# Performance work log

Measured on AMD Instinct MI355X. Metric: run time of the kernel, lower is better.

The kernel has to match this reference:

```python
import jax, jax.numpy as jnp
import numpy as np

EMB = 768
HEADS = 12


def setup_inputs() -> dict:
    key = jax.random.key(0)
    ks = jax.random.split(key, 5)
    B, N, E = 8, 1024, EMB
    x = jax.random.normal(ks[0], (B, N, E), dtype=jnp.float32)
    s = 1.0 / np.sqrt(E)
    W_qkv = jax.random.normal(ks[1], (E, 3 * E), dtype=jnp.float32) * s
    b_qkv = jnp.zeros((3 * E,), dtype=jnp.float32)
    W_fc = jax.random.normal(ks[2], (E, E), dtype=jnp.float32) * s
    b_fc = jnp.zeros((E,), dtype=jnp.float32)
    return {"x": x, "W_qkv": W_qkv, "b_qkv": b_qkv, "W_fc": W_fc, "b_fc": b_fc}


def reference(x, W_qkv, b_qkv, W_fc, b_fc):
    B, N, E = x.shape
    H = HEADS
    D = E // H
    qkv = x @ W_qkv + b_qkv                      # [B, N, 3E]
    q, k, v = jnp.split(qkv, 3, axis=-1)
    # b n (h d) -> b h n d
    def to_heads(t):
        return t.reshape(B, N, H, D).transpose(0, 2, 1, 3)
    q, k, v = to_heads(q), to_heads(k), to_heads(v)
    scale = 1.0 / jnp.sqrt(jnp.float32(E))       # NOTE: scales by sqrt(emb_size), not head dim
    attn = jnp.einsum('bhid,bhjd->bhij', q, k) * scale
    attn = jax.nn.softmax(attn, axis=-1)
    out = jnp.einsum('bhij,bhjd->bhid', attn, v)
    out = out.transpose(0, 2, 1, 3).reshape(B, N, E)  # b h n d -> b n (h d)
    return out @ W_fc + b_fc
```

## Files before the change

### kernel.cpp

```cpp
#include <hip/hip_runtime.h>
#include <hip/hip_bf16.h>


typedef unsigned short u16;
typedef unsigned int u32;
typedef __attribute__((ext_vector_type(8))) short short8;
typedef __attribute__((ext_vector_type(4))) float f32x4;

#define DEV static __device__ __forceinline__

DEV u16 f2bf(float f) {
  union { float f; u32 u; } v; v.f = f;
  return (u16)((v.u + 0x7FFFu + ((v.u >> 16) & 1u)) >> 16);
}

DEV u32 pk2(float lo, float hi) {
  union { __hip_bfloat162 h2; u32 u; } v;
  v.h2.x = __float2bfloat16(lo);
  v.h2.y = __float2bfloat16(hi);
  return v.u;
}

DEV void gload_lds16(const void* g, void* l) {
  __builtin_amdgcn_global_load_lds(
      (const __attribute__((address_space(1))) void*)g,
      (__attribute__((address_space(3))) void*)l, 16, 0, 0);
}

__global__ void prep_kernel(const float* __restrict__ x, u16* __restrict__ xb,
                            const float* __restrict__ Wq, u16* __restrict__ WqT,
                            const float* __restrict__ Wf, u16* __restrict__ WfT) {
  __shared__ u16 tile[64][72];
  const int b = blockIdx.x;
  const int t = threadIdx.x;
  if (b < 576) {
    const float* in;
    u16* out;
    int Nn, bid;
    if (b < 432) { in = Wq; out = WqT; Nn = 2304; bid = b; }
    else         { in = Wf; out = WfT; Nn = 768;  bid = b - 432; }
    const int K = 768;
    int ntiles = Nn >> 6;
    int tk = bid / ntiles, tn = bid % ntiles;
    int k0 = tk << 6, n0 = tn << 6;
    int r = t >> 4;
    int c4 = (t & 15) << 2;
#pragma unroll
    for (int ps = 0; ps < 4; ++ps) {
      int k = r + ps * 16;
      float4 v = *reinterpret_cast<const float4*>(&in[(size_t)(k0 + k) * Nn + n0 + c4]);
      tile[c4 + 0][k] = f2bf(v.x);
      tile[c4 + 1][k] = f2bf(v.y);
      tile[c4 + 2][k] = f2bf(v.z);
      tile[c4 + 3][k] = f2bf(v.w);
    }
    __syncthreads();
    int nr = t >> 3;
    int c8 = (t & 7) << 3;
#pragma unroll
    for (int ps = 0; ps < 2; ++ps) {
      int n = nr + ps * 32;
      uint4 v = *reinterpret_cast<const uint4*>(&tile[n][c8]);
      *reinterpret_cast<uint4*>(&out[(size_t)(n0 + n) * K + k0 + c8]) = v;
    }
  } else {
    const int n8 = (8192 * 768) / 8;
    int idx = (b - 576) * 256 + t;
    const int stride = 2048 * 256;
    for (int i = idx; i < n8; i += stride) {
      float4 a = reinterpret_cast<const float4*>(x)[2 * i];
      float4 c = reinterpret_cast<const float4*>(x)[2 * i + 1];
      uint4 o;
      o.x = f2bf(a.x) | ((u32)f2bf(a.y) << 16);
      o.y = f2bf(a.z) | ((u32)f2bf(a.w) << 16);
      o.z = f2bf(c.x) | ((u32)f2bf(c.y) << 16);
      o.w = f2bf(c.z) | ((u32)f2bf(c.w) << 16);
      reinterpret_cast<uint4*>(xb)[i] = o;
    }
  }
}

template <int MODE>
__global__ __launch_bounds__(256, 4) void gemm_bt(
    const u16* __restrict__ A, const u16* __restrict__ Bt,
    const float* __restrict__ bias, void* __restrict__ Cout,
    u16* __restrict__ qh, u16* __restrict__ kh, u16* __restrict__ vt,
    int Nn) {
  __shared__ u16 SMEM[17408];
  u16* const As0 = SMEM;
  u16* const As1 = SMEM + 4096;
  u16* const Bs0 = SMEM + 8192;
  u16* const Bs1 = SMEM + 12288;
  const int nTn = Nn >> 7;
  const int nwg = gridDim.x;
  int wg = blockIdx.x;
  wg = (wg & 7) * (nwg >> 3) + (wg >> 3);
  const int tm = wg / nTn, tn = wg % nTn;
  const int m0 = tm << 7, n0 = tn << 7;
  const int tid = threadIdx.x;
  const int w = tid >> 6, lane = tid & 63;
  const int g = lane >> 4, p = lane & 15;
  const int wr = w >> 1, wc = w & 1;

  const int srow = lane >> 2;
  const int schunk = (lane & 3) ^ ((srow >> 1) & 3);
  const u16* Asrc = A + (size_t)(m0 + srow) * 768 + schunk * 8;
  const u16* Bsrc = Bt + (size_t)(n0 + srow) * 768 + schunk * 8;
  const int csw = (g ^ ((p >> 1) & 3)) << 3;

  f32x4 acc[4][4] = {};

#define STAGE(kt, ap, bp)                                                       \
  do {                                                                          \
    _Pragma("unroll")                                                           \
    for (int i = 0; i < 2; ++i) {                                               \
      int trow = w * 32 + i * 16;                                               \
      gload_lds16(Asrc + (size_t)trow * 768 + (kt) * 32, (ap) + trow * 32);     \
      gload_lds16(Bsrc + (size_t)trow * 768 + (kt) * 32, (bp) + trow * 32);     \
    }                                                                           \
  } while (0)

  STAGE(0, As0, Bs0);
  __syncthreads();

  int buf = 0;
  for (int k = 0; k < 24; ++k) {
    const u16* as = buf ? As1 : As0;
    const u16* bs = buf ? Bs1 : Bs0;
    short8 af[4], bf[4];
#pragma unroll
    for (int mb = 0; mb < 4; ++mb)
      af[mb] = *reinterpret_cast<const short8*>(&as[(wr * 64 + mb * 16 + p) * 32 + csw]);
#pragma unroll
    for (int nb = 0; nb < 4; ++nb)
      bf[nb] = *reinterpret_cast<const short8*>(&bs[(wc * 64 + nb * 16 + p) * 32 + csw]);
    if (k < 23) STAGE(k + 1, buf ? As0 : As1, buf ? Bs0 : Bs1);
#pragma unroll
    for (int mb = 0; mb < 4; ++mb)
#pragma unroll
      for (int nb = 0; nb < 4; ++nb)
        acc[mb][nb] = __builtin_amdgcn_mfma_f32_16x16x32_bf16(af[mb], bf[nb], acc[mb][nb], 0, 0, 0);
    __syncthreads();
    buf ^= 1;
  }
#undef STAGE

  const float qscale = 0.05205878290161879f;
  if (MODE == 0) {
#pragma unroll
    for (int nb = 0; nb < 4; ++nb) {
      int ncol = n0 + wc * 64 + nb * 16 + p;
      float bv = bias[ncol];
#pragma unroll
      for (int mb = 0; mb < 4; ++mb)
#pragma unroll
        for (int r = 0; r < 4; ++r) {
          int m = m0 + wr * 64 + mb * 16 + g * 4 + r;
          ((float*)Cout)[(size_t)m * Nn + ncol] = acc[mb][nb][r] + bv;
        }
    }
  } else if (n0 < 1536) {
#pragma unroll
    for (int nb = 0; nb < 4; ++nb) {
      int ncol = n0 + wc * 64 + nb * 16 + p;
      float bv = bias[ncol];
      int h64 = ncol >> 6;
      int which = h64 / 12;
      int hh = h64 - which * 12;
      int d = ncol & 63;
      u16* dst = which == 0 ? qh : kh;
      float sc = which == 0 ? qscale : 1.f;
#pragma unroll
      for (int mb = 0; mb < 4; ++mb)
#pragma unroll
        for (int r = 0; r < 4; ++r) {
          int m = m0 + wr * 64 + mb * 16 + g * 4 + r;
          int bb = m >> 10, nr = m & 1023;
          dst[(((size_t)bb * 12 + hh) * 1024 + nr) * 64 + d] = f2bf((acc[mb][nb][r] + bv) * sc);
        }
    }
  } else {
#pragma unroll
    for (int nb = 0; nb < 4; ++nb) {
      int nl = wc * 64 + nb * 16 + p;
      float bv = bias[n0 + nl];
#pragma unroll
      for (int mb = 0; mb < 4; ++mb) {
        int mlb = wr * 64 + mb * 16 + g * 4;
        uint2 pkv;
        pkv.x = (u32)f2bf(acc[mb][nb][0] + bv) | ((u32)f2bf(acc[mb][nb][1] + bv) << 16);
        pkv.y = (u32)f2bf(acc[mb][nb][2] + bv) | ((u32)f2bf(acc[mb][nb][3] + bv) << 16);
        *reinterpret_cast<uint2*>(&SMEM[nl * 136 + mlb]) = pkv;
      }
    }
    __syncthreads();
    const int hhb = (n0 - 1536) >> 6;
    const int bb = m0 >> 10;
    const int nseq0 = m0 & 1023;
    const int c16 = (tid & 7) * 16;
#pragma unroll
    for (int ps = 0; ps < 4; ++ps) {
      int nl = (tid >> 3) + ps * 32;
      int hh = hhb + (nl >> 6);
      int d = nl & 63;
      u16* dst = vt + (((size_t)(bb * 12 + hh) * 64 + d) << 10) + nseq0 + c16;
      uint4 v0 = *reinterpret_cast<const uint4*>(&SMEM[nl * 136 + c16]);
      uint4 v1 = *reinterpret_cast<const uint4*>(&SMEM[nl * 136 + c16 + 8]);
      *reinterpret_cast<uint4*>(dst) = v0;
      *reinterpret_cast<uint4*>(dst + 8) = v1;
    }
  }
}

__global__ __launch_bounds__(512, 6) void attn_kernel(
    const u16* __restrict__ qh, const u16* __restrict__ kh,
    const u16* __restrict__ vt, u16* __restrict__ ao) {
  __shared__ u16 Ks[2][64 * 64];
  __shared__ u16 Vs[2][64 * 64];
  __shared__ u16 Ps[8][16 * 64];
  const int bid = blockIdx.x;
  const int qt = bid & 7;
  const int bh = bid >> 3;
  const int b = bh / 12, h = bh % 12;
  const int tid = threadIdx.x;
  const int w = tid >> 6, lane = tid & 63;
  const int g = lane >> 4, p = lane & 15;
  const int qrow = qt * 128 + w * 16;

  const u16* qbase = qh + ((size_t)bh * 1024 + qrow + p) * 64;
  short8 qf0 = *reinterpret_cast<const short8*>(qbase + g * 8);
  short8 qf1 = *reinterpret_cast<const short8*>(qbase + 32 + g * 8);

  const int ci = w * 64 + lane;
  const int crow = ci >> 3;
  const int csw = (ci & 7) ^ (crow & 7);
  const u16* ksrc = kh + (((size_t)bh * 1024 + crow) << 6) + csw * 8;
  const u16* vsrc = vt + ((size_t)bh * 64 + crow) * 1024 + csw * 8;
  u16* myp = Ps[w];

  const int sw = p & 7;
  const int c0 = (g ^ sw) << 3;
  const int c1 = ((4 + g) ^ sw) << 3;

  float m_run = -1e30f, l_run = 0.f;
  f32x4 oacc[4] = {};

  gload_lds16(ksrc, &Ks[0][w * 512]);
  gload_lds16(vsrc, &Vs[0][w * 512]);
  __syncthreads();

  int buf = 0;
  for (int kt = 0; kt < 1024; kt += 64) {
    if (kt < 960) {
      gload_lds16(ksrc + ((kt + 64) << 6), &Ks[buf ^ 1][w * 512]);
      gload_lds16(vsrc + (kt + 64), &Vs[buf ^ 1][w * 512]);
    }

    f32x4 s[4];
    __builtin_amdgcn_s_setprio(1);
#pragma unroll
    for (int jb = 0; jb < 4; ++jb) {
      const u16* kb = &Ks[buf][(jb * 16 + p) * 64];
      short8 k0 = *reinterpret_cast<const short8*>(kb + c0);
      short8 k1 = *reinterpret_cast<const short8*>(kb + c1);
      f32x4 z = {};
      z = __builtin_amdgcn_mfma_f32_16x16x32_bf16(k0, qf0, z, 0, 0, 0);
      z = __builtin_amdgcn_mfma_f32_16x16x32_bf16(k1, qf1, z, 0, 0, 0);
      s[jb] = z;
    }
    __builtin_amdgcn_s_setprio(0);

    float tmax = -1e30f;
#pragma unroll
    for (int jb = 0; jb < 4; ++jb)
#pragma unroll
      for (int r = 0; r < 4; ++r) tmax = fmaxf(tmax, s[jb][r]);
    tmax = fmaxf(tmax, __shfl_xor(tmax, 16));
    tmax = fmaxf(tmax, __shfl_xor(tmax, 32));

    if (!__all(tmax - m_run <= 8.f)) {
      float m_new = fmaxf(m_run, tmax);
      float alpha = __builtin_amdgcn_exp2f(m_run - m_new);
      float al[4];
#pragma unroll
      for (int r = 0; r < 4; ++r) al[r] = __shfl(alpha, g * 4 + r);
#pragma unroll
      for (int nb = 0; nb < 4; ++nb)
#pragma unroll
        for (int r = 0; r < 4; ++r) oacc[nb][r] *= al[r];
      l_run *= alpha;
      m_run = m_new;
    }

    float lsum = 0.f;
#pragma unroll
    for (int jb = 0; jb < 4; ++jb)
#pragma unroll
      for (int r = 0; r < 4; ++r) {
        float e = __builtin_amdgcn_exp2f(s[jb][r] - m_run);
        s[jb][r] = e;
        lsum += e;
      }
    lsum += __shfl_xor(lsum, 16);
    lsum += __shfl_xor(lsum, 32);
    l_run += lsum;

#pragma unroll
    for (int jb = 0; jb < 4; ++jb) {
      uint2 pkv;
      pkv.x = pk2(s[jb][0], s[jb][1]);
      pkv.y = pk2(s[jb][2], s[jb][3]);
      int c = 2 * jb + (g >> 1);
      *reinterpret_cast<uint2*>(&myp[p * 64 + ((c ^ sw) << 3) + ((g & 1) << 2)]) = pkv;
    }

    short8 pa0 = *reinterpret_cast<const short8*>(&myp[p * 64 + c0]);
    short8 pa1 = *reinterpret_cast<const short8*>(&myp[p * 64 + c1]);
    __builtin_amdgcn_s_setprio(1);
#pragma unroll
    for (int nb = 0; nb < 4; ++nb) {
      const u16* vb = &Vs[buf][(nb * 16 + p) * 64];
      short8 v0 = *reinterpret_cast<const short8*>(vb + c0);
      short8 v1 = *reinterpret_cast<const short8*>(vb + c1);
      oacc[nb] = __builtin_amdgcn_mfma_f32_16x16x32_bf16(pa0, v0, oacc[nb], 0, 0, 0);
      oacc[nb] = __builtin_amdgcn_mfma_f32_16x16x32_bf16(pa1, v1, oacc[nb], 0, 0, 0);
    }
    __builtin_amdgcn_s_setprio(0);

    __syncthreads();
    buf ^= 1;
  }

  float li[4];
#pragma unroll
  for (int r = 0; r < 4; ++r) li[r] = 1.f / __shfl(l_run, g * 4 + r);
  u16* obase = ao + ((size_t)(b * 1024 + qrow)) * 768 + h * 64;
#pragma unroll
  for (int nb = 0; nb < 4; ++nb)
#pragma unroll
    for (int r = 0; r < 4; ++r)
      obase[(size_t)(g * 4 + r) * 768 + nb * 16 + p] = f2bf(oacc[nb][r] * li[r]);
}

extern "C" void kernel_launch(void* const* d_in, const int* in_sizes, int n_in,
                              void* d_out, int out_size, void* d_ws, size_t ws_size,
                              hipStream_t stream) {
  const float* x = (const float*)d_in[0];
  const float* Wqkv = (const float*)d_in[1];
  const float* bqkv = (const float*)d_in[2];
  const float* Wfc = (const float*)d_in[3];
  const float* bfc = (const float*)d_in[4];
  float* out = (float*)d_out;

  char* ws = (char*)d_ws;
  u16* xb    = (u16*)(ws);
  u16* wqkvT = (u16*)(ws + 12582912);
  u16* wfcT  = (u16*)(ws + 16121856);
  u16* qh    = (u16*)(ws + 17301504);
  u16* kh    = (u16*)(ws + 29884416);
  u16* vt    = (u16*)(ws + 55050240);
  u16* ao    = (u16*)(ws + 67633152);

  prep_kernel<<<2624, 256, 0, stream>>>(x, xb, Wqkv, wqkvT, Wfc, wfcT);
  gemm_bt<2><<<64 * 18, 256, 0, stream>>>(xb, wqkvT, bqkv, nullptr, qh, kh, vt, 2304);
  attn_kernel<<<96 * 8, 512, 0, stream>>>(qh, kh, vt, ao);
  gemm_bt<0><<<64 * 6, 256, 0, stream>>>(ao, wfcT, bfc, out, nullptr, nullptr, nullptr, 768);
}
```

Measured before the change: 124.1 us.

## Read K and V tiles directly from global memory instead of LDS double buffer

```diff
diff --git a/kernel.cpp b/kernel.cpp
--- a/kernel.cpp
+++ b/kernel.cpp
@@ -212,11 +212,9 @@
   }
 }
 
-__global__ __launch_bounds__(512, 6) void attn_kernel(
+__global__ __launch_bounds__(512, 4) void attn_kernel(
     const u16* __restrict__ qh, const u16* __restrict__ kh,
     const u16* __restrict__ vt, u16* __restrict__ ao) {
-  __shared__ u16 Ks[2][64 * 64];
-  __shared__ u16 Vs[2][64 * 64];
   __shared__ u16 Ps[8][16 * 64];
   const int bid = blockIdx.x;
   const int qt = bid & 7;
@@ -231,11 +229,8 @@
   short8 qf0 = *reinterpret_cast<const short8*>(qbase + g * 8);
   short8 qf1 = *reinterpret_cast<const short8*>(qbase + 32 + g * 8);
 
-  const int ci = w * 64 + lane;
-  const int crow = ci >> 3;
-  const int csw = (ci & 7) ^ (crow & 7);
-  const u16* ksrc = kh + (((size_t)bh * 1024 + crow) << 6) + csw * 8;
-  const u16* vsrc = vt + ((size_t)bh * 64 + crow) * 1024 + csw * 8;
+  const u16* kbase = kh + ((size_t)bh * 1024 + p) * 64;
+  const u16* vbase = vt + ((size_t)bh * 64 + p) * 1024;
   u16* myp = Ps[w];
 
   const int sw = p & 7;
@@ -245,30 +240,18 @@
   float m_run = -1e30f, l_run = 0.f;
   f32x4 oacc[4] = {};
 
-  gload_lds16(ksrc, &Ks[0][w * 512]);
-  gload_lds16(vsrc, &Vs[0][w * 512]);
-  __syncthreads();
-
-  int buf = 0;
   for (int kt = 0; kt < 1024; kt += 64) {
-    if (kt < 960) {
-      gload_lds16(ksrc + ((kt + 64) << 6), &Ks[buf ^ 1][w * 512]);
-      gload_lds16(vsrc + (kt + 64), &Vs[buf ^ 1][w * 512]);
-    }
-
     f32x4 s[4];
-    __builtin_amdgcn_s_setprio(1);
 #pragma unroll
     for (int jb = 0; jb < 4; ++jb) {
-      const u16* kb = &Ks[buf][(jb * 16 + p) * 64];
-      short8 k0 = *reinterpret_cast<const short8*>(kb + c0);
-      short8 k1 = *reinterpret_cast<const short8*>(kb + c1);
+      const u16* kr = kbase + (size_t)(kt + jb * 16) * 64;
+      short8 k0 = *reinterpret_cast<const short8*>(kr + g * 8);
+      short8 k1 = *reinterpret_cast<const short8*>(kr + 32 + g * 8);
       f32x4 z = {};
       z = __builtin_amdgcn_mfma_f32_16x16x32_bf16(k0, qf0, z, 0, 0, 0);
       z = __builtin_amdgcn_mfma_f32_16x16x32_bf16(k1, qf1, z, 0, 0, 0);
       s[jb] = z;
     }
-    __builtin_amdgcn_s_setprio(0);
 
     float tmax = -1e30f;
 #pragma unroll
@@ -316,19 +299,14 @@
 
     short8 pa0 = *reinterpret_cast<const short8*>(&myp[p * 64 + c0]);
     short8 pa1 = *reinterpret_cast<const short8*>(&myp[p * 64 + c1]);
-    __builtin_amdgcn_s_setprio(1);
 #pragma unroll
     for (int nb = 0; nb < 4; ++nb) {
-      const u16* vb = &Vs[buf][(nb * 16 + p) * 64];
-      short8 v0 = *reinterpret_cast<const short8*>(vb + c0);
-      short8 v1 = *reinterpret_cast<const short8*>(vb + c1);
+      const u16* vr = vbase + (size_t)(nb * 16) * 1024 + kt;
+      short8 v0 = *reinterpret_cast<const short8*>(vr + g * 8);
+      short8 v1 = *reinterpret_cast<const short8*>(vr + 32 + g * 8);
       oacc[nb] = __builtin_amdgcn_mfma_f32_16x16x32_bf16(pa0, v0, oacc[nb], 0, 0, 0);
       oacc[nb] = __builtin_amdgcn_mfma_f32_16x16x32_bf16(pa1, v1, oacc[nb], 0, 0, 0);
     }
-    __builtin_amdgcn_s_setprio(0);
-
-    __syncthreads();
-    buf ^= 1;
   }
 
   float li[4];
```

Result: slower. 248.9 us (+100.7%).
